# Optimization experiments

Hardware: AMD Instinct MI355X
Metric: run time of the kernel (lower is better)

## Reference

```python
import jax, jax.numpy as jnp
import numpy as np

B, S, H, NH = 4, 1024, 1024, 16
DH = H // NH
EPS = 1e-12  # BERT layer_norm_eps


def layer_norm(x, scale, bias, eps=EPS):
    mu = jnp.mean(x, axis=-1, keepdims=True)
    var = jnp.var(x, axis=-1, keepdims=True)
    return (x - mu) / jnp.sqrt(var + eps) * scale + bias


def setup_inputs() -> dict:
    key = jax.random.key(0)
    ks = jax.random.split(key, 8)
    lin = lambda k: jax.random.normal(k, (H, H), jnp.float32) * 0.02
    zeros_h = jnp.zeros((H,), jnp.float32)
    return {
        "hidden_states": jax.random.normal(ks[0], (B, S, H), jnp.float32),
        "group_prob": jnp.zeros((B, S, S), jnp.float32),
        "attention_mask": jnp.ones((B, 1, S, S), jnp.int32),
        "Wq": lin(ks[1]), "bq": zeros_h,
        "Wk": lin(ks[2]), "bk": zeros_h,
        "Wv": lin(ks[3]), "bv": zeros_h,
        "gWq": lin(ks[4]), "gbq": zeros_h,
        "gWk": lin(ks[5]), "gbk": zeros_h,
        "g_ln_scale": jnp.ones((H,), jnp.float32), "g_ln_bias": zeros_h,
        "Wo": lin(ks[6]), "bo": zeros_h,
        "out_ln_scale": jnp.ones((H,), jnp.float32), "out_ln_bias": zeros_h,
    }


def _forward(hidden_states, group_prob, attention_mask, Wq, bq, Wk, bk, Wv, bv,
             gWq, gbq, gWk, gbk, g_ln_scale, g_ln_bias, Wo, bo,
             out_ln_scale, out_ln_bias):
    am = attention_mask.astype(jnp.int32)              # [B,1,S,S]
    a = jnp.eye(S, k=1, dtype=jnp.int32)               # superdiagonal
    b = jnp.eye(S, dtype=jnp.int32)                    # identity
    c = jnp.eye(S, k=-1, dtype=jnp.int32)              # subdiagonal
    tri = jnp.triu(jnp.ones((S, S), jnp.float32))      # upper tri incl diag

    # ---- GroupAttention (tree-transformer constituent priors) ----
    hs = layer_norm(hidden_states, g_ln_scale, g_ln_bias)
    gq = hs @ gWq.T + gbq
    gk = hs @ gWk.T + gbk
    g_scores = jnp.einsum('bqd,bkd->bqk', gq, gk) / jnp.float32(H)
    g_mask = (am & (a + c))[:, 0]                      # [B,S,S] tridiag band, no diag
    g_scores = jnp.where(g_mask == 0, -jnp.inf, g_scores)
    n_attn = jnp.nan_to_num(jax.nn.softmax(g_scores, axis=-1))
    n_attn = jnp.sqrt(n_attn * jnp.swapaxes(n_attn, -1, -2) + 1e-9)
    n_attn = group_prob + (1.0 - group_prob) * n_attn  # prior mixing
    t = jnp.where(a == 0, 0.0, jnp.log(n_attn + 1e-9)) @ tri
    g_attn = jnp.exp(tri @ t)
    strict_upper = tri.astype(jnp.int32) - b           # nonzero on strict upper tri
    g_attn = jnp.where(strict_upper == 0, 0.0, g_attn)
    g_attn = g_attn + jnp.swapaxes(g_attn, -1, -2) + jnp.where(b == 0, 1e-9, n_attn)
    break_prob = n_attn

    # ---- BertSelfAttention, mode 'L' ----
    def split_heads(x):
        return x.reshape(B, S, NH, DH).transpose(0, 2, 1, 3)  # [B,NH,S,DH]
    q = split_heads(hidden_states @ Wq.T + bq)
    k = split_heads(hidden_states @ Wk.T + bk)
    v = split_heads(hidden_states @ Wv.T + bv)
    scores = jnp.einsum('bhqd,bhkd->bhqk', q, k) / jnp.sqrt(jnp.float32(DH))
    keep = (am | b) != 0                               # diag always attended
    scores = jnp.where(keep, scores, -jnp.inf)
    probs = jax.nn.softmax(scores, axis=-1)
    probs = probs * g_attn[:, None]                    # group-prob reweighting
    ctx = jnp.einsum('bhqk,bhkd->bhqd', probs, v)
    ctx = ctx.transpose(0, 2, 1, 3).reshape(B, S, H)

    # ---- BertSelfOutput: dense + residual + LayerNorm ----
    out = layer_norm(ctx @ Wo.T + bo + hidden_states, out_ln_scale, out_ln_bias)
    return out, scores, g_attn, break_prob


def reference(hidden_states, group_prob, attention_mask, Wq, bq, Wk, bk, Wv, bv,
              gWq, gbq, gWk, gbk, g_ln_scale, g_ln_bias, Wo, bo,
              out_ln_scale, out_ln_bias):
    return _forward(hidden_states, group_prob, attention_mask, Wq, bq, Wk, bk,
                    Wv, bv, gWq, gbq, gWk, gbk, g_ln_scale, g_ln_bias, Wo, bo,
                    out_ln_scale, out_ln_bias)
```

## Files before the change

kernel.cpp:

```cpp
#include <hip/hip_runtime.h>
#include <math.h>

#define BB 4
#define S 1024
#define H 1024
#define NHD 16
#define DH 64
#define LN_EPS 1e-12f
#define SQ9 3.1622776601683795e-5f
#define NEG_INF (-__builtin_inff())
#define L2E 1.4426950408889634f

typedef unsigned short u16;
typedef unsigned int u32;
using bfrag = __attribute__((ext_vector_type(8))) short;
using f32x4 = __attribute__((ext_vector_type(4))) float;

typedef __attribute__((address_space(1))) void void_g;
typedef __attribute__((address_space(3))) void void_l;

__device__ __forceinline__ void gload16(const void* g, void* l) {
  __builtin_amdgcn_global_load_lds((void_g*)g, (void_l*)l, 16, 0, 0);
}

__device__ __forceinline__ u16 f2bf(float f) {
  u32 u = __builtin_bit_cast(u32, f);
  u32 r = (u + 0x7fffu + ((u >> 16) & 1u)) >> 16;
  return (u16)r;
}
__device__ __forceinline__ float bf2f(u32 b) {
  u32 u = b << 16;
  return __builtin_bit_cast(float, u);
}

__device__ __forceinline__ float block_sum256(float v, float* buf) {
#pragma unroll
  for (int o = 32; o > 0; o >>= 1) v += __shfl_down(v, o);
  if ((threadIdx.x & 63) == 0) buf[threadIdx.x >> 6] = v;
  __syncthreads();
  float r = buf[0] + buf[1] + buf[2] + buf[3];
  __syncthreads();
  return r;
}

__global__ __launch_bounds__(256) void prep_kernel(
    const float* __restrict__ Wq, const float* __restrict__ Wk, const float* __restrict__ Wv,
    const float* __restrict__ gWq, const float* __restrict__ gWk,
    const float* __restrict__ hidden, const int* __restrict__ am,
    const float* __restrict__ glns, const float* __restrict__ glnb,
    u16* __restrict__ dstW, u32* __restrict__ amb, u16* __restrict__ hsbf) {
  __shared__ float buf[4];
  int bid = blockIdx.x;
  if (bid < 9216) {
    const int WQ = 262144;
    int i = bid * 256 + threadIdx.x;
    const float* src; int off;
    if      (i < 1 * WQ) { src = Wq;  off = 0; }
    else if (i < 2 * WQ) { src = Wk;  off = 1 * WQ; }
    else if (i < 3 * WQ) { src = Wv;  off = 2 * WQ; }
    else if (i < 4 * WQ) { src = gWq; off = 3 * WQ; }
    else if (i < 5 * WQ) { src = gWk; off = 4 * WQ; }
    else                 { src = hidden; off = 5 * WQ; }
    float4 v = reinterpret_cast<const float4*>(src)[i - off];
    u32 lo = (u32)f2bf(v.x) | ((u32)f2bf(v.y) << 16);
    u32 hi = (u32)f2bf(v.z) | ((u32)f2bf(v.w) << 16);
    reinterpret_cast<uint2*>(dstW)[i] = make_uint2(lo, hi);
  } else if (bid < 25600) {
    size_t t = (size_t)(bid - 9216) * 256 + threadIdx.x;
    int v = am[t] != 0;
    unsigned long long m = __ballot(v);
    int lane = threadIdx.x & 63;
    if (lane == 0)       amb[t >> 5] = (u32)m;
    else if (lane == 32) amb[t >> 5] = (u32)(m >> 32);
  } else {
    size_t row = bid - 25600;
    const float4 xv = reinterpret_cast<const float4*>(hidden + row * H)[threadIdx.x];
    float s  = xv.x + xv.y + xv.z + xv.w;
    float s2 = xv.x * xv.x + xv.y * xv.y + xv.z * xv.z + xv.w * xv.w;
    s  = block_sum256(s, buf);
    s2 = block_sum256(s2, buf);
    float mu  = s * (1.0f / H);
    float var = s2 * (1.0f / H) - mu * mu;
    float inv = rsqrtf(var + LN_EPS);
    const float4 sv = reinterpret_cast<const float4*>(glns)[threadIdx.x];
    const float4 bv = reinterpret_cast<const float4*>(glnb)[threadIdx.x];
    float o0 = (xv.x - mu) * inv * sv.x + bv.x;
    float o1 = (xv.y - mu) * inv * sv.y + bv.y;
    float o2 = (xv.z - mu) * inv * sv.z + bv.z;
    float o3 = (xv.w - mu) * inv * sv.w + bv.w;
    u32 lo = (u32)f2bf(o0) | ((u32)f2bf(o1) << 16);
    u32 hi = (u32)f2bf(o2) | ((u32)f2bf(o3) << 16);
    reinterpret_cast<uint2*>(hsbf + row * H)[threadIdx.x] = make_uint2(lo, hi);
  }
}

__global__ __launch_bounds__(256) void cast_wo_kernel(const float* __restrict__ Wo,
                                                      u16* __restrict__ dst) {
  int i = blockIdx.x * 256 + threadIdx.x;
  float4 v = reinterpret_cast<const float4*>(Wo)[i];
  u32 lo = (u32)f2bf(v.x) | ((u32)f2bf(v.y) << 16);
  u32 hi = (u32)f2bf(v.z) | ((u32)f2bf(v.w) << 16);
  reinterpret_cast<uint2*>(dst)[i] = make_uint2(lo, hi);
}

__global__ __launch_bounds__(256) void mega_gemm(
    const u16* __restrict__ hbf, const u16* __restrict__ hsbf,
    const u16* __restrict__ Wcat,
    const float* __restrict__ bq, const float* __restrict__ bk, const float* __restrict__ bv,
    const float* __restrict__ gbq, const float* __restrict__ gbk,
    u16* __restrict__ q, u16* __restrict__ k, u16* __restrict__ vt,
    u16* __restrict__ gq, u16* __restrict__ gk) {
  __shared__ __align__(16) u16 SM[32768];
  const int Kdim = H;
  int fid = blockIdx.x + blockIdx.y * 40;
  int swz = (fid & 7) * 160 + (fid >> 3);
  int lx = swz % 40, ly = swz / 40;
  int which = lx >> 3;
  const u16* A = (which < 3) ? hbf : hsbf;
  int rowBlk = ly * 128, colBlk = lx * 128;
  int tid = threadIdx.x, wid = tid >> 6, l = tid & 63;
  int dr = l >> 3, sl = l & 7;
  int co = (sl ^ dr) << 3;
  const u16* Ag = A + (size_t)rowBlk * Kdim;
  const u16* Bg = Wcat + (size_t)colBlk * Kdim;
  f32x4 acc[4][4];
#pragma unroll
  for (int i = 0; i < 4; ++i)
#pragma unroll
    for (int j = 0; j < 4; ++j) acc[i][j] = (f32x4){0.f, 0.f, 0.f, 0.f};
#pragma unroll
  for (int i = 0; i < 4; ++i) {
    int L = wid * 4 + i;
    gload16(Ag + (size_t)(L * 8 + dr) * Kdim + co, &SM[L * 512]);
    gload16(Bg + (size_t)(L * 8 + dr) * Kdim + co, &SM[16384 + L * 512]);
  }
  __syncthreads();
  int wm = wid >> 1, wn = wid & 1;
  const int nt = Kdim >> 6;
  int buf = 0;
  int sw = (l & 7) << 4;
  for (int t = 0; t < nt; ++t) {
    if (t + 1 < nt) {
      int k0 = (t + 1) << 6;
      int dstoff = (buf ^ 1) * 8192;
#pragma unroll
      for (int i = 0; i < 4; ++i) {
        int L = wid * 4 + i;
        gload16(Ag + (size_t)(L * 8 + dr) * Kdim + k0 + co, &SM[dstoff + L * 512]);
        gload16(Bg + (size_t)(L * 8 + dr) * Kdim + k0 + co, &SM[16384 + dstoff + L * 512]);
      }
    }
    const char* Ab = (const char*)&SM[buf * 8192];
    const char* Bb = (const char*)&SM[16384 + buf * 8192];
#pragma unroll
    for (int ks = 0; ks < 2; ++ks) {
      int kb = (ks * 64 + ((l >> 4) << 4)) ^ sw;
      bfrag af[4], bfv[4];
#pragma unroll
      for (int mi = 0; mi < 4; ++mi)
        af[mi] = *(const bfrag*)(Ab + (wm * 64 + mi * 16 + (l & 15)) * 128 + kb);
#pragma unroll
      for (int ni = 0; ni < 4; ++ni)
        bfv[ni] = *(const bfrag*)(Bb + (wn * 64 + ni * 16 + (l & 15)) * 128 + kb);
#pragma unroll
      for (int mi = 0; mi < 4; ++mi)
#pragma unroll
        for (int ni = 0; ni < 4; ++ni)
          acc[mi][ni] = __builtin_amdgcn_mfma_f32_16x16x32_bf16(af[mi], bfv[ni], acc[mi][ni], 0, 0, 0);
    }
    __syncthreads();
    buf ^= 1;
  }
  const float* bias = (which == 0) ? bq : (which == 1) ? bk : (which == 2) ? bv
                      : (which == 3) ? gbq : gbk;
  if (which == 2) {
    u16* T = SM;
#pragma unroll
    for (int mi = 0; mi < 4; ++mi) {
#pragma unroll
      for (int ni = 0; ni < 4; ++ni) {
        int c = wn * 64 + ni * 16 + (l & 15);
        float bvv = bias[(colBlk & 1023) + c];
        int tokb = wm * 64 + mi * 16 + ((l >> 4) << 2);
        u32 w0 = (u32)f2bf(acc[mi][ni][0] + bvv) | ((u32)f2bf(acc[mi][ni][1] + bvv) << 16);
        u32 w1 = (u32)f2bf(acc[mi][ni][2] + bvv) | ((u32)f2bf(acc[mi][ni][3] + bvv) << 16);
        *(u32*)&T[c * 144 + tokb]     = w0;
        *(u32*)&T[c * 144 + tokb + 2] = w1;
      }
    }
    __syncthreads();
    int col = tid >> 1, th = tid & 1;
    int g = (colBlk & 1023) + col;
    int bb = rowBlk >> 10;
    int s0 = (rowBlk & 1023) + th * 64;
    const uint4* src = (const uint4*)&T[col * 144 + th * 64];
    u16* dst = vt + ((size_t)(bb * 1024 + g)) * S + s0;
#pragma unroll
    for (int i = 0; i < 8; ++i) reinterpret_cast<uint4*>(dst)[i] = src[i];
  } else {
    u16* O = (which == 0) ? q : (which == 1) ? k : (which == 3) ? gq : gk;
#pragma unroll
    for (int mi = 0; mi < 4; ++mi) {
#pragma unroll
      for (int ni = 0; ni < 4; ++ni) {
        int col = (colBlk + wn * 64 + ni * 16 + (l & 15)) & 1023;
        float bvv = bias[col];
#pragma unroll
        for (int j = 0; j < 4; ++j) {
          int row = rowBlk + wm * 64 + mi * 16 + ((l >> 4) << 2) + j;
          O[(size_t)row * H + col] = f2bf(acc[mi][ni][j] + bvv);
        }
      }
    }
  }
}

__global__ __launch_bounds__(256) void gemm_dense(
    const u16* __restrict__ A, const u16* __restrict__ Bw,
    const float* __restrict__ bias, const float* __restrict__ resid,
    u16* __restrict__ C) {
  __shared__ __align__(16) u16 SM[32768];
  const int Kdim = H;
  int fid = blockIdx.x + blockIdx.y * 8;
  int swz = (fid & 7) * 32 + (fid >> 3);
  int lx = swz & 7, ly = swz >> 3;
  int rowBlk = ly * 128, colBlk = lx * 128;
  int tid = threadIdx.x, wid = tid >> 6, l = tid & 63;
  int dr = l >> 3, sl = l & 7;
  int co = (sl ^ dr) << 3;
  const u16* Ag = A + (size_t)rowBlk * Kdim;
  const u16* Bg = Bw + (size_t)colBlk * Kdim;
  f32x4 acc[4][4];
#pragma unroll
  for (int i = 0; i < 4; ++i)
#pragma unroll
    for (int j = 0; j < 4; ++j) acc[i][j] = (f32x4){0.f, 0.f, 0.f, 0.f};
#pragma unroll
  for (int i = 0; i < 4; ++i) {
    int L = wid * 4 + i;
    gload16(Ag + (size_t)(L * 8 + dr) * Kdim + co, &SM[L * 512]);
    gload16(Bg + (size_t)(L * 8 + dr) * Kdim + co, &SM[16384 + L * 512]);
  }
  __syncthreads();
  int wm = wid >> 1, wn = wid & 1;
  const int nt = Kdim >> 6;
  int buf = 0;
  int sw = (l & 7) << 4;
  for (int t = 0; t < nt; ++t) {
    if (t + 1 < nt) {
      int k0 = (t + 1) << 6;
      int dstoff = (buf ^ 1) * 8192;
#pragma unroll
      for (int i = 0; i < 4; ++i) {
        int L = wid * 4 + i;
        gload16(Ag + (size_t)(L * 8 + dr) * Kdim + k0 + co, &SM[dstoff + L * 512]);
        gload16(Bg + (size_t)(L * 8 + dr) * Kdim + k0 + co, &SM[16384 + dstoff + L * 512]);
      }
    }
    const char* Ab = (const char*)&SM[buf * 8192];
    const char* Bb = (const char*)&SM[16384 + buf * 8192];
#pragma unroll
    for (int ks = 0; ks < 2; ++ks) {
      int kb = (ks * 64 + ((l >> 4) << 4)) ^ sw;
      bfrag af[4], bfv[4];
#pragma unroll
      for (int mi = 0; mi < 4; ++mi)
        af[mi] = *(const bfrag*)(Ab + (wm * 64 + mi * 16 + (l & 15)) * 128 + kb);
#pragma unroll
      for (int ni = 0; ni < 4; ++ni)
        bfv[ni] = *(const bfrag*)(Bb + (wn * 64 + ni * 16 + (l & 15)) * 128 + kb);
#pragma unroll
      for (int mi = 0; mi < 4; ++mi)
#pragma unroll
        for (int ni = 0; ni < 4; ++ni)
          acc[mi][ni] = __builtin_amdgcn_mfma_f32_16x16x32_bf16(af[mi], bfv[ni], acc[mi][ni], 0, 0, 0);
    }
    __syncthreads();
    buf ^= 1;
  }
#pragma unroll
  for (int mi = 0; mi < 4; ++mi) {
#pragma unroll
    for (int ni = 0; ni < 4; ++ni) {
      int col = colBlk + wn * 64 + ni * 16 + (l & 15);
      float bvv = bias[col];
#pragma unroll
      for (int j = 0; j < 4; ++j) {
        int row = rowBlk + wm * 64 + mi * 16 + ((l >> 4) << 2) + j;
        C[(size_t)row * H + col] = f2bf(acc[mi][ni][j] + bvv + resid[(size_t)row * H + col]);
      }
    }
  }
}

__global__ __launch_bounds__(256) void band_dots_kernel(
    const u16* __restrict__ gq, const u16* __restrict__ gk,
    float* __restrict__ znext, float* __restrict__ zprev) {
  __shared__ float buf[4];
  size_t idx = blockIdx.x;
  int i = (int)(idx & (S - 1));
  uint2 q2 = reinterpret_cast<const uint2*>(gq + idx * H)[threadIdx.x];
  float q0 = bf2f(q2.x & 0xffff), q1 = bf2f(q2.x >> 16);
  float q2f = bf2f(q2.y & 0xffff), q3 = bf2f(q2.y >> 16);
  float dn = 0.f, dp = 0.f;
  if (i < S - 1) {
    uint2 k2 = reinterpret_cast<const uint2*>(gk + (idx + 1) * H)[threadIdx.x];
    dn = q0 * bf2f(k2.x & 0xffff) + q1 * bf2f(k2.x >> 16) +
         q2f * bf2f(k2.y & 0xffff) + q3 * bf2f(k2.y >> 16);
  }
  if (i > 0) {
    uint2 k2 = reinterpret_cast<const uint2*>(gk + (idx - 1) * H)[threadIdx.x];
    dp = q0 * bf2f(k2.x & 0xffff) + q1 * bf2f(k2.x >> 16) +
         q2f * bf2f(k2.y & 0xffff) + q3 * bf2f(k2.y >> 16);
  }
  dn = block_sum256(dn, buf);
  dp = block_sum256(dp, buf);
  if (threadIdx.x == 0) { znext[idx] = dn; zprev[idx] = dp; }
}

__global__ __launch_bounds__(1024) void band_prefix_kernel(
    const float* __restrict__ znext, const float* __restrict__ zprev,
    const int* __restrict__ am, const float* __restrict__ gp,
    float* __restrict__ sband, float* __restrict__ Cpre) {
  __shared__ float pd[S];
  __shared__ float scn[S];
  int b = blockIdx.x, i = threadIdx.x;
  size_t idx = (size_t)b * S + i;
  bool luv = (i < S - 1) && (am[((size_t)b * S + i) * S + i + 1] != 0);
  bool ldv = (i > 0) && (am[((size_t)b * S + i) * S + i - 1] != 0);
  float pf, pdn;
  if (!luv && !ldv) { pf = 0.f; pdn = 0.f; }
  else if (!ldv)    { pf = 1.f; pdn = 0.f; }
  else if (!luv)    { pf = 0.f; pdn = 1.f; }
  else {
    float lu = znext[idx] * (1.0f / (float)H);
    float ld = zprev[idx] * (1.0f / (float)H);
    float m = fmaxf(lu, ld);
    float eu = expf(lu - m), ed = expf(ld - m);
    float inv = 1.f / (eu + ed);
    pf = eu * inv; pdn = ed * inv;
  }
  pd[i] = pdn;
  __syncthreads();
  float sb = 0.f, L = 0.f;
  if (i < S - 1) {
    sb = sqrtf(pf * pd[i + 1] + 1e-9f);
    float gpv = gp[((size_t)b * S + i) * S + (i + 1)];
    float nm = gpv + (1.f - gpv) * sb;
    L = logf(nm + 1e-9f);
  }
  sband[idx] = sb;
  scn[i] = L;
  __syncthreads();
  for (int off = 1; off < S; off <<= 1) {
    float t = (i >= off) ? scn[i - off] : 0.f;
    __syncthreads();
    scn[i] += t;
    __syncthreads();
  }
  Cpre[idx] = (i > 0) ? scn[i - 1] : 0.f;
}

__global__ __launch_bounds__(256) void gattn_write_kernel(
    const float* __restrict__ gp, const float* __restrict__ sband,
    const float* __restrict__ Cpre, float* __restrict__ ga, float* __restrict__ brk) {
  __shared__ float Crow[S];
  __shared__ float Srow[S];
  size_t bi = blockIdx.x;
  int b = (int)(bi >> 10), i = (int)(bi & (S - 1));
  reinterpret_cast<float4*>(Crow)[threadIdx.x] =
      reinterpret_cast<const float4*>(Cpre + (size_t)b * S)[threadIdx.x];
  reinterpret_cast<float4*>(Srow)[threadIdx.x] =
      reinterpret_cast<const float4*>(sband + (size_t)b * S)[threadIdx.x];
  __syncthreads();
  float Ci = Crow[i];
  size_t rowoff = bi * S;
  const float4 g4 = reinterpret_cast<const float4*>(gp + rowoff)[threadIdx.x];
  const float gparr[4] = {g4.x, g4.y, g4.z, g4.w};
  float go[4], bo_[4];
#pragma unroll
  for (int j = 0; j < 4; ++j) {
    int k = threadIdx.x * 4 + j;
    float gpv = gparr[j];
    float gav;
    if (k == i) {
      gav = gpv + (1.f - gpv) * SQ9;
    } else {
      float d = (k > i) ? (Crow[k] - Ci) : (Ci - Crow[k]);
      gav = expf(d) + 1e-9f;
    }
    float sval = (k == i + 1) ? Srow[i] : ((k == i - 1) ? Srow[k] : SQ9);
    go[j]  = gav;
    bo_[j] = gpv + (1.f - gpv) * sval;
  }
  f32x4 go4 = (f32x4){go[0], go[1], go[2], go[3]};
  __builtin_nontemporal_store(go4, reinterpret_cast<f32x4*>(ga + rowoff) + threadIdx.x);
  f32x4 bo4 = (f32x4){bo_[0], bo_[1], bo_[2], bo_[3]};
  __builtin_nontemporal_store(bo4, reinterpret_cast<f32x4*>(brk + rowoff) + threadIdx.x);
}

__global__ __launch_bounds__(512) void flash_kernel(
    const u16* __restrict__ q, const u16* __restrict__ k, const u16* __restrict__ vt,
    const u32* __restrict__ amb, const float* __restrict__ Cpre,
    const float* __restrict__ gp,
    float* __restrict__ scores, u16* __restrict__ ctx) {
  __shared__ __align__(16) u16 QPt[8192];
  __shared__ __align__(16) u16 Kt[2][4096];
  __shared__ __align__(16) u16 Vt[2][4096];
  __shared__ float CLds[1024];
  int fid = blockIdx.x + blockIdx.y * 8;
  int qb = (fid >> 3) & 7;
  int bh = (fid & 7) * 8 + (fid >> 6);
  int b = bh >> 4, h = bh & 15;
  int tid = threadIdx.x, wid = tid >> 6, l = tid & 63;
  int dr = l >> 3, sl = l & 7;
  int co = (sl ^ dr) << 3;
  const u16* qbase = q + ((size_t)b * S + qb * 128) * H + h * 64;
  const u16* kbase = k + (size_t)b * S * H + h * 64;
  const u16* vtb   = vt + (size_t)bh * 64 * S;
  {
    float2 c2 = reinterpret_cast<const float2*>(Cpre + (size_t)b * S)[tid];
    c2.x *= L2E; c2.y *= L2E;
    reinterpret_cast<float2*>(CLds)[tid] = c2;
  }
#pragma unroll
  for (int i = 0; i < 2; ++i) {
    int L = wid * 2 + i;
    gload16(qbase + (size_t)(L * 8 + dr) * H + co, &QPt[L * 512]);
  }
  gload16(kbase + (size_t)(wid * 8 + dr) * H + co, &Kt[0][wid * 512]);
  gload16(vtb + (size_t)(wid * 8 + dr) * S + co, &Vt[0][wid * 512]);
  __syncthreads();
  int sw = (l & 7) << 4;
  int qr = l & 15;
  bfrag qa[2];
#pragma unroll
  for (int ks = 0; ks < 2; ++ks) {
    int kb = (ks * 64 + ((l >> 4) << 4)) ^ sw;
    qa[ks] = *(const bfrag*)((const char*)QPt + (wid * 16 + qr) * 128 + kb);
  }
  __syncthreads();
  int rowg0 = qb * 128 + wid * 16 + ((l >> 4) << 2);
  float Ci2[4], gdiag[4];
#pragma unroll
  for (int j = 0; j < 4; ++j) {
    int row = rowg0 + j;
    Ci2[j] = CLds[row];
    float gpd = gp[((size_t)b * S + row) * S + row];
    gdiag[j] = gpd + (1.f - gpd) * SQ9;
  }
  float m_run[4], l_loc[4];
  f32x4 oacc[4];
#pragma unroll
  for (int j = 0; j < 4; ++j) { m_run[j] = NEG_INF; l_loc[j] = 0.f; }
#pragma unroll
  for (int nb = 0; nb < 4; ++nb) oacc[nb] = (f32x4){0.f, 0.f, 0.f, 0.f};
  int cur = 0;
  for (int kt = 0; kt < 16; ++kt) {
    if (kt < 15) {
      gload16(kbase + (size_t)((kt + 1) * 64 + wid * 8 + dr) * H + co, &Kt[cur ^ 1][wid * 512]);
      gload16(vtb + (size_t)(wid * 8 + dr) * S + (kt + 1) * 64 + co, &Vt[cur ^ 1][wid * 512]);
    }
    f32x4 acc[4];
#pragma unroll
    for (int nb = 0; nb < 4; ++nb) acc[nb] = (f32x4){0.f, 0.f, 0.f, 0.f};
    __builtin_amdgcn_s_setprio(1);
#pragma unroll
    for (int ks = 0; ks < 2; ++ks) {
      int kb = (ks * 64 + ((l >> 4) << 4)) ^ sw;
#pragma unroll
      for (int nb = 0; nb < 4; ++nb) {
        bfrag bv = *(const bfrag*)((const char*)Kt[cur] + (nb * 16 + qr) * 128 + kb);
        acc[nb] = __builtin_amdgcn_mfma_f32_16x16x32_bf16(qa[ks], bv, acc[nb], 0, 0, 0);
      }
    }
    __builtin_amdgcn_s_setprio(0);
    float vals[4][4];
    float tm[4] = {NEG_INF, NEG_INF, NEG_INF, NEG_INF};
#pragma unroll
    for (int j = 0; j < 4; ++j) {
      int row = rowg0 + j;
      uint2 w01 = *reinterpret_cast<const uint2*>(amb + ((size_t)b * S + row) * 32 + kt * 2);
      float* srow = scores + ((size_t)bh * S + row) * S + kt * 64;
#pragma unroll
      for (int nb = 0; nb < 4; ++nb) {
        int col = nb * 16 + qr;
        int colg = kt * 64 + col;
        u32 word = (nb < 2) ? w01.x : w01.y;
        int keep = (int)((word >> (col & 31)) & 1u) | (row == colg);
        float v = keep ? acc[nb][j] * 0.125f : NEG_INF;
        vals[nb][j] = v;
        __builtin_nontemporal_store(v, srow + col);
        tm[j] = fmaxf(tm[j], v);
      }
    }
#pragma unroll
    for (int j = 0; j < 4; ++j) {
#pragma unroll
      for (int o = 1; o < 16; o <<= 1) tm[j] = fmaxf(tm[j], __shfl_xor(tm[j], o));
    }
    float Ck2[4];
#pragma unroll
    for (int nb = 0; nb < 4; ++nb) Ck2[nb] = CLds[kt * 64 + nb * 16 + qr];
#pragma unroll
    for (int j = 0; j < 4; ++j) {
      int row = rowg0 + j;
      int prow = wid * 16 + ((l >> 4) << 2) + j;
      char* ptrow = (char*)QPt + prow * 128;
      int psw = (prow & 7) << 4;
      float mn = fmaxf(m_run[j], tm[j]);
      float pp[4], pg[4];
      float sc;
      if (mn > NEG_INF) {
        sc = exp2f((m_run[j] - mn) * L2E);
        float m2 = mn * L2E;
#pragma unroll
        for (int nb = 0; nb < 4; ++nb) {
          float t = __builtin_fmaf(vals[nb][j], L2E, -m2);
          pp[nb] = exp2f(t);
          int colg = kt * 64 + nb * 16 + qr;
          float d2 = (colg > row) ? (Ck2[nb] - Ci2[j]) : (Ci2[j] - Ck2[nb]);
          float g = exp2f(t + d2);
          pg[nb] = (colg == row) ? pp[nb] * gdiag[j] : g;
        }
      } else {
        sc = 1.f;
#pragma unroll
        for (int nb = 0; nb < 4; ++nb) { pp[nb] = 0.f; pg[nb] = 0.f; }
      }
      m_run[j] = mn;
      l_loc[j] = l_loc[j] * sc + (pp[0] + pp[1] + pp[2] + pp[3]);
#pragma unroll
      for (int nb = 0; nb < 4; ++nb) {
        *(u16*)(ptrow + (((nb * 16 + qr) * 2) ^ psw)) = f2bf(pg[nb]);
        oacc[nb][j] *= sc;
      }
    }
    __builtin_amdgcn_s_setprio(1);
#pragma unroll
    for (int ks = 0; ks < 2; ++ks) {
      int kb = (ks * 64 + ((l >> 4) << 4)) ^ sw;
      bfrag pa = *(const bfrag*)((const char*)QPt + (wid * 16 + qr) * 128 + kb);
#pragma unroll
      for (int nb = 0; nb < 4; ++nb) {
        bfrag vv = *(const bfrag*)((const char*)Vt[cur] + (nb * 16 + qr) * 128 + kb);
        oacc[nb] = __builtin_amdgcn_mfma_f32_16x16x32_bf16(pa, vv, oacc[nb], 0, 0, 0);
      }
    }
    __builtin_amdgcn_s_setprio(0);
    __syncthreads();
    cur ^= 1;
  }
#pragma unroll
  for (int j = 0; j < 4; ++j) {
#pragma unroll
    for (int o = 1; o < 16; o <<= 1) l_loc[j] += __shfl_xor(l_loc[j], o);
  }
#pragma unroll
  for (int j = 0; j < 4; ++j) {
    int row = rowg0 + j;
    float ir = 1.f / l_loc[j];
#pragma unroll
    for (int nb = 0; nb < 4; ++nb) {
      int d = nb * 16 + qr;
      ctx[((size_t)b * S + row) * H + h * 64 + d] = f2bf(oacc[nb][j] * ir);
    }
  }
}

__global__ __launch_bounds__(256) void ln_bf_kernel(
    const u16* __restrict__ x, const float* __restrict__ sc,
    const float* __restrict__ bi, float* __restrict__ y) {
  __shared__ float buf[4];
  size_t row = blockIdx.x;
  uint2 xv = reinterpret_cast<const uint2*>(x + row * H)[threadIdx.x];
  float x0 = bf2f(xv.x & 0xffff), x1 = bf2f(xv.x >> 16);
  float x2 = bf2f(xv.y & 0xffff), x3 = bf2f(xv.y >> 16);
  float s  = x0 + x1 + x2 + x3;
  float s2 = x0 * x0 + x1 * x1 + x2 * x2 + x3 * x3;
  s  = block_sum256(s, buf);
  s2 = block_sum256(s2, buf);
  float mu  = s * (1.0f / H);
  float var = s2 * (1.0f / H) - mu * mu;
  float inv = rsqrtf(var + LN_EPS);
  const float4 sv = reinterpret_cast<const float4*>(sc)[threadIdx.x];
  const float4 bv = reinterpret_cast<const float4*>(bi)[threadIdx.x];
  float4 o;
  o.x = (x0 - mu) * inv * sv.x + bv.x;
  o.y = (x1 - mu) * inv * sv.y + bv.y;
  o.z = (x2 - mu) * inv * sv.z + bv.z;
  o.w = (x3 - mu) * inv * sv.w + bv.w;
  reinterpret_cast<float4*>(y + row * H)[threadIdx.x] = o;
}

extern "C" void kernel_launch(void* const* d_in, const int* in_sizes, int n_in,
                              void* d_out, int out_size, void* d_ws, size_t ws_size,
                              hipStream_t stream) {
  const float* hidden = (const float*)d_in[0];
  const float* gp     = (const float*)d_in[1];
  const int*   am     = (const int*)d_in[2];
  const float* Wq = (const float*)d_in[3];  const float* bq = (const float*)d_in[4];
  const float* Wk = (const float*)d_in[5];  const float* bk = (const float*)d_in[6];
  const float* Wv = (const float*)d_in[7];  const float* bv = (const float*)d_in[8];
  const float* gWq = (const float*)d_in[9]; const float* gbq = (const float*)d_in[10];
  const float* gWk = (const float*)d_in[11];const float* gbk = (const float*)d_in[12];
  const float* glns = (const float*)d_in[13]; const float* glnb = (const float*)d_in[14];
  const float* Wo = (const float*)d_in[15]; const float* bo = (const float*)d_in[16];
  const float* olns = (const float*)d_in[17]; const float* olnb = (const float*)d_in[18];

  float* out    = (float*)d_out;
  float* scores = out + (size_t)BB * S * H;
  float* gattn  = scores + (size_t)BB * NHD * S * S;
  float* brk    = gattn + (size_t)BB * S * S;

  const size_t MB = 1u << 20;
  char* w = (char*)d_ws;
  u16* Wcat  = (u16*)(w);
  u16* hbf   = (u16*)(w + 10 * MB);
  u16* ctxbf = hbf;
  u16* hsbf  = (u16*)(w + 18 * MB);
  u16* Wobf  = hsbf;
  u16* qbf   = (u16*)(w + 26 * MB);
  u16* kbf   = (u16*)(w + 34 * MB);
  u16* vtb   = (u16*)(w + 42 * MB);
  u16* gqbf  = (u16*)(w + 50 * MB);
  u16* densebf = gqbf;
  u16* gkbf  = (u16*)(w + 58 * MB);
  u32* amb   = (u32*)(w + 66 * MB);
  float* znext  = (float*)(w + 66 * MB + 512 * 1024);
  float* zprev  = znext + BB * S;
  float* sbandA = zprev + BB * S;
  float* CpreA  = sbandA + BB * S;

  dim3 blk(256);

  prep_kernel<<<29696, blk, 0, stream>>>(Wq, Wk, Wv, gWq, gWk, hidden, am,
                                         glns, glnb, Wcat, amb, hsbf);

  mega_gemm<<<dim3(40, 32), blk, 0, stream>>>(hbf, hsbf, Wcat,
                                              bq, bk, bv, gbq, gbk,
                                              qbf, kbf, vtb, gqbf, gkbf);
  cast_wo_kernel<<<1024, blk, 0, stream>>>(Wo, Wobf);

  band_dots_kernel<<<BB * S, blk, 0, stream>>>(gqbf, gkbf, znext, zprev);
  band_prefix_kernel<<<BB, 1024, 0, stream>>>(znext, zprev, am, gp, sbandA, CpreA);
  gattn_write_kernel<<<BB * S, blk, 0, stream>>>(gp, sbandA, CpreA, gattn, brk);

  flash_kernel<<<dim3(8, 64), dim3(512), 0, stream>>>(qbf, kbf, vtb, amb, CpreA,
                                                      gp, scores, ctxbf);

  gemm_dense<<<dim3(8, 32), blk, 0, stream>>>(ctxbf, Wobf, bo, hidden, densebf);
  ln_bf_kernel<<<BB * S, blk, 0, stream>>>(densebf, olns, olnb, out);
}
```

Baseline: 261.0 us.

## Fuse Wo cast into band_dots, lazy softmax rescale, relax flash loop barrier

Three separate changes. The Wo fp32-to-bf16 cast moves into extra blocks of band_dots_kernel, which removes one kernel launch. The flash kernel's online softmax now rescales only when the new tile max exceeds the running max by more than 8, so most tiles skip the exp and multiply on the accumulators. The per-iteration __syncthreads is replaced by a partial vmcnt wait plus a raw s_barrier, so outstanding global loads can stay in flight across the barrier. The lazy rescale lets unnormalized exponentials grow up to about e^8 before the final division by l_loc, and the partial wait risks LDS hazards if the wait count is wrong.

```diff
diff --git a/kernel.cpp b/kernel.cpp
--- a/kernel.cpp
+++ b/kernel.cpp
@@ -94,15 +94,6 @@
   }
 }
 
-__global__ __launch_bounds__(256) void cast_wo_kernel(const float* __restrict__ Wo,
-                                                      u16* __restrict__ dst) {
-  int i = blockIdx.x * 256 + threadIdx.x;
-  float4 v = reinterpret_cast<const float4*>(Wo)[i];
-  u32 lo = (u32)f2bf(v.x) | ((u32)f2bf(v.y) << 16);
-  u32 hi = (u32)f2bf(v.z) | ((u32)f2bf(v.w) << 16);
-  reinterpret_cast<uint2*>(dst)[i] = make_uint2(lo, hi);
-}
-
 __global__ __launch_bounds__(256) void mega_gemm(
     const u16* __restrict__ hbf, const u16* __restrict__ hsbf,
     const u16* __restrict__ Wcat,
@@ -295,9 +286,19 @@
 
 __global__ __launch_bounds__(256) void band_dots_kernel(
     const u16* __restrict__ gq, const u16* __restrict__ gk,
+    const float* __restrict__ Wo, u16* __restrict__ Wobf,
     float* __restrict__ znext, float* __restrict__ zprev) {
   __shared__ float buf[4];
-  size_t idx = blockIdx.x;
+  int bid = blockIdx.x;
+  if (bid >= 4096) {
+    int i = (bid - 4096) * 256 + threadIdx.x;
+    float4 v = reinterpret_cast<const float4*>(Wo)[i];
+    u32 lo = (u32)f2bf(v.x) | ((u32)f2bf(v.y) << 16);
+    u32 hi = (u32)f2bf(v.z) | ((u32)f2bf(v.w) << 16);
+    reinterpret_cast<uint2*>(Wobf)[i] = make_uint2(lo, hi);
+    return;
+  }
+  size_t idx = bid;
   int i = (int)(idx & (S - 1));
   uint2 q2 = reinterpret_cast<const uint2*>(gq + idx * H)[threadIdx.x];
   float q0 = bf2f(q2.x & 0xffff), q1 = bf2f(q2.x >> 16);
@@ -508,11 +509,16 @@
       int prow = wid * 16 + ((l >> 4) << 2) + j;
       char* ptrow = (char*)QPt + prow * 128;
       int psw = (prow & 7) << 4;
-      float mn = fmaxf(m_run[j], tm[j]);
+      if (tm[j] > m_run[j] + 8.0f) {
+        float sc = exp2f((m_run[j] - tm[j]) * L2E);
+        m_run[j] = tm[j];
+        l_loc[j] *= sc;
+#pragma unroll
+        for (int nb = 0; nb < 4; ++nb) oacc[nb][j] *= sc;
+      }
+      float mn = m_run[j];
       float pp[4], pg[4];
-      float sc;
       if (mn > NEG_INF) {
-        sc = exp2f((m_run[j] - mn) * L2E);
         float m2 = mn * L2E;
 #pragma unroll
         for (int nb = 0; nb < 4; ++nb) {
@@ -524,17 +530,13 @@
           pg[nb] = (colg == row) ? pp[nb] * gdiag[j] : g;
         }
       } else {
-        sc = 1.f;
 #pragma unroll
         for (int nb = 0; nb < 4; ++nb) { pp[nb] = 0.f; pg[nb] = 0.f; }
       }
-      m_run[j] = mn;
-      l_loc[j] = l_loc[j] * sc + (pp[0] + pp[1] + pp[2] + pp[3]);
-#pragma unroll
-      for (int nb = 0; nb < 4; ++nb) {
+      l_loc[j] += pp[0] + pp[1] + pp[2] + pp[3];
+#pragma unroll
+      for (int nb = 0; nb < 4; ++nb)
         *(u16*)(ptrow + (((nb * 16 + qr) * 2) ^ psw)) = f2bf(pg[nb]);
-        oacc[nb][j] *= sc;
-      }
     }
     __builtin_amdgcn_s_setprio(1);
 #pragma unroll
@@ -548,7 +550,9 @@
       }
     }
     __builtin_amdgcn_s_setprio(0);
-    __syncthreads();
+    asm volatile("s_waitcnt vmcnt(16)" ::: "memory");
+    __builtin_amdgcn_s_barrier();
+    __builtin_amdgcn_sched_barrier(0);
     cur ^= 1;
   }
 #pragma unroll
@@ -640,9 +644,8 @@
   mega_gemm<<<dim3(40, 32), blk, 0, stream>>>(hbf, hsbf, Wcat,
                                               bq, bk, bv, gbq, gbk,
                                               qbf, kbf, vtb, gqbf, gkbf);
-  cast_wo_kernel<<<1024, blk, 0, stream>>>(Wo, Wobf);
-
-  band_dots_kernel<<<BB * S, blk, 0, stream>>>(gqbf, gkbf, znext, zprev);
+
+  band_dots_kernel<<<5120, blk, 0, stream>>>(gqbf, gkbf, Wo, Wobf, znext, zprev);
   band_prefix_kernel<<<BB, 1024, 0, stream>>>(znext, zprev, am, gp, sbandA, CpreA);
   gattn_write_kernel<<<BB * S, blk, 0, stream>>>(gp, sbandA, CpreA, gattn, brk);
 
```

Result: faster. 246.3 us (-5.6%).
